# Kernel tuning notes

Hardware: AMD Instinct MI355X
Metric: run time of the kernel (lower is better)

Reference implementation:

```python
import jax, jax.numpy as jnp
import numpy as np

BETA = 0.25

def _l2norm(x, eps=1e-12):
    # F.normalize(x, dim=-1)
    n = jnp.sqrt(jnp.sum(x * x, axis=-1, keepdims=True))
    return x / jnp.maximum(n, eps)

def setup_inputs() -> dict:
    key = jax.random.key(0)
    k1, k2 = jax.random.split(key)
    z = jax.random.normal(k1, (32, 1024, 32), dtype=jnp.float32)
    embedding = jax.random.normal(k2, (8192, 32), dtype=jnp.float32)
    return {"z": z, "embedding": embedding}

def reference(z, embedding):
    B, T, D = z.shape
    zf = _l2norm(z.reshape(-1, D))            # [N, D]
    en = _l2norm(embedding)                   # [n_e, D]
    # squared distances: ||z||^2 + ||e||^2 - 2 z.e  -> [N, n_e]
    d = (jnp.sum(zf * zf, axis=1, keepdims=True)
         + jnp.sum(en * en, axis=1)
         - 2.0 * jnp.einsum('nd,kd->nk', zf, en))
    idx = jnp.argmin(d, axis=1).reshape(B, T)            # [B, T]
    z_q = embedding[idx]                                  # [B, T, D] gather
    z_qnorm = _l2norm(z_q)
    z_norm = _l2norm(z)
    loss = (BETA * jnp.mean((jax.lax.stop_gradient(z_qnorm) - z_norm) ** 2)
            + jnp.mean((z_qnorm - jax.lax.stop_gradient(z_norm)) ** 2))
    # straight-through estimator
    z_q_out = z + jax.lax.stop_gradient(z_qnorm - z)
    return z_q_out, loss, idx
```

## Files before the change

### kernel.cpp

```cpp
#include <hip/hip_runtime.h>
#include <math.h>


#define D 32
#define KCODES 8192
#define MARGIN 2.5e-4f
#define EPS 1e-12f

typedef short bf16x8 __attribute__((ext_vector_type(8)));
typedef unsigned short u16x8 __attribute__((ext_vector_type(8)));
typedef float f32x4 __attribute__((ext_vector_type(4)));

static __device__ __forceinline__ unsigned short f2bf(float x) {
  unsigned u = __float_as_uint(x);
  return (unsigned short)((u + 0x7FFFu + ((u >> 16) & 1u)) >> 16);
}
static __device__ __forceinline__ float bf2f(unsigned short s) {
  return __uint_as_float(((unsigned)s) << 16);
}
static __device__ __forceinline__ void gload_lds16(const void* g, void* l) {
  __builtin_amdgcn_global_load_lds(
      (const __attribute__((address_space(1))) void*)g,
      (__attribute__((address_space(3))) void*)l, 16, 0, 0);
}


__global__ __launch_bounds__(256) void k_prep(const float* __restrict__ z,
                                              const float* __restrict__ emb,
                                              float* __restrict__ en,
                                              float* __restrict__ en_h,
                                              unsigned short* __restrict__ eswz,
                                              unsigned short* __restrict__ zswz_hi,
                                              unsigned short* __restrict__ zswz_lo,
                                              float* __restrict__ zn,
                                              int* __restrict__ cnt,
                                              float* __restrict__ loss,
                                              unsigned long long* __restrict__ mp2,
                                              int N) {
  int v = blockIdx.x * 256 + threadIdx.x;
  if (v == 0) { *cnt = 0; *loss = 0.f; }
  if (v >= KCODES + N) return;
  if (v >= KCODES) mp2[v - KCODES] = 0ull;
  const float* src = (v < KCODES) ? (emb + (size_t)v * D) : (z + (size_t)(v - KCODES) * D);

  float x[D];
  const float4* p = reinterpret_cast<const float4*>(src);
#pragma unroll
  for (int j = 0; j < D / 4; ++j) {
    float4 q = p[j];
    x[4 * j + 0] = q.x; x[4 * j + 1] = q.y; x[4 * j + 2] = q.z; x[4 * j + 3] = q.w;
  }
  float ss = 0.f;
#pragma unroll
  for (int j = 0; j < D; ++j) ss = fmaf(x[j], x[j], ss);
  float n = fmaxf(sqrtf(ss), EPS);
#pragma unroll
  for (int j = 0; j < D; ++j) x[j] = x[j] / n;

  unsigned short hi[D], lo[D];
#pragma unroll
  for (int j = 0; j < D; ++j) {
    hi[j] = f2bf(x[j]);
    lo[j] = f2bf(x[j] - bf2f(hi[j]));
  }

  if (v < KCODES) {
    float4* o = reinterpret_cast<float4*>(en + (size_t)v * D);
    float s2 = 0.f;
#pragma unroll
    for (int j = 0; j < D / 4; ++j) {
      float4 q = {x[4 * j], x[4 * j + 1], x[4 * j + 2], x[4 * j + 3]};
      s2 = fmaf(q.x, q.x, fmaf(q.y, q.y, fmaf(q.z, q.z, fmaf(q.w, q.w, s2))));
      o[j] = q;
    }
    en_h[v] = 0.5f * s2;
    int tl = v >> 4, m = v & 15;
#pragma unroll
    for (int q = 0; q < 4; ++q) {
      u16x8 hv, lv;
#pragma unroll
      for (int j = 0; j < 8; ++j) { hv[j] = hi[8 * q + j]; lv[j] = lo[8 * q + j]; }
      *(u16x8*)(eswz + (size_t)tl * 1024 + (q * 16 + m) * 8) = hv;
      *(u16x8*)(eswz + (size_t)tl * 1024 + 512 + (q * 16 + m) * 8) = lv;
    }
  } else {
    int r = v - KCODES;
    float4* zo = reinterpret_cast<float4*>(zn + (size_t)r * D);
#pragma unroll
    for (int j = 0; j < D / 4; ++j) {
      float4 q = {x[4 * j], x[4 * j + 1], x[4 * j + 2], x[4 * j + 3]};
      zo[j] = q;
    }
    int g = r >> 4, m = r & 15;
#pragma unroll
    for (int q = 0; q < 4; ++q) {
      u16x8 hv, lv;
#pragma unroll
      for (int j = 0; j < 8; ++j) { hv[j] = hi[8 * q + j]; lv[j] = lo[8 * q + j]; }
      *(u16x8*)(zswz_hi + (size_t)g * 512 + (q * 16 + m) * 8) = hv;
      *(u16x8*)(zswz_lo + (size_t)g * 512 + (q * 16 + m) * 8) = lv;
    }
  }
}

__global__ __launch_bounds__(256, 4) void k_argmin_mfma(
    const unsigned short* __restrict__ zswz_hi,
    const unsigned short* __restrict__ zswz_lo,
    const unsigned short* __restrict__ eswz,
    float* __restrict__ res_s1, int* __restrict__ res_cb,
    float* __restrict__ res_s2) {
  __shared__ unsigned short lds_sh[2][8192];

  const int tid = threadIdx.x;
  const int wid = tid >> 6, lane = tid & 63;
  const int lane15 = lane & 15, quad = lane >> 4;
  const int rs = blockIdx.x >> 2;
  const int qt = blockIdx.x & 3;

  bf16x8 zhi[4], zlo[4];
#pragma unroll
  for (int rg = 0; rg < 4; ++rg) {
    int g = rs * 16 + wid * 4 + rg;
    zhi[rg] = *(const bf16x8*)(zswz_hi + (size_t)g * 512 + lane * 8);
    zlo[rg] = *(const bf16x8*)(zswz_lo + (size_t)g * 512 + lane * 8);
  }

  float cm[4], s1g[4], s2c[4];
  int cb[4];
#pragma unroll
  for (int rg = 0; rg < 4; ++rg) {
    cm[rg] = -3.4e38f; s1g[rg] = -3.4e38f; s2c[rg] = -3.4e38f; cb[rg] = 0;
  }
  const f32x4 zero4 = {0.f, 0.f, 0.f, 0.f};

  const float4* gall = reinterpret_cast<const float4*>(eswz) + (size_t)qt * 16 * 1024;
#pragma unroll
  for (int i = 0; i < 4; ++i) {
    int off = i * 256 + tid;
    gload_lds16(gall + off, (char*)&lds_sh[0][0] + (size_t)off * 16);
  }

  for (int c = 0; c < 16; ++c) {
    __syncthreads();
    if (c + 1 < 16) {
      const float4* gn = gall + (size_t)(c + 1) * 1024;
      char* dst = (char*)&lds_sh[(c + 1) & 1][0];
#pragma unroll
      for (int i = 0; i < 4; ++i) {
        int off = i * 256 + tid;
        gload_lds16(gn + off, dst + (size_t)off * 16);
      }
    }
    const unsigned short* buf = &lds_sh[c & 1][0];
#pragma unroll
    for (int t = 0; t < 8; ++t) {
      bf16x8 ahi = *(const bf16x8*)(buf + t * 1024 + lane * 8);
      bf16x8 alo = *(const bf16x8*)(buf + t * 1024 + 512 + lane * 8);
#pragma unroll
      for (int rg = 0; rg < 4; ++rg) {
        f32x4 acc = __builtin_amdgcn_mfma_f32_16x16x32_bf16(ahi, zhi[rg], zero4, 0, 0, 0);
        acc = __builtin_amdgcn_mfma_f32_16x16x32_bf16(ahi, zlo[rg], acc, 0, 0, 0);
        acc = __builtin_amdgcn_mfma_f32_16x16x32_bf16(alo, zhi[rg], acc, 0, 0, 0);
        cm[rg] = fmaxf(cm[rg],
                       fmaxf(fmaxf(acc[0], acc[1]), fmaxf(acc[2], acc[3])));
      }
    }
#pragma unroll
    for (int rg = 0; rg < 4; ++rg) {
      float old1 = s1g[rg];
      s2c[rg] = fmaxf(s2c[rg], fminf(cm[rg], old1));
      bool better = cm[rg] > old1;
      cb[rg] = better ? ((qt * 16 + c) >> 1) : cb[rg];
      s1g[rg] = better ? cm[rg] : old1;
      cm[rg] = -3.4e38f;
    }
  }

#pragma unroll
  for (int m = 16; m <= 32; m <<= 1) {
#pragma unroll
    for (int rg = 0; rg < 4; ++rg) {
      float o1 = __shfl_xor(s1g[rg], m, 64);
      float o2 = __shfl_xor(s2c[rg], m, 64);
      int ob = __shfl_xor(cb[rg], m, 64);
      s2c[rg] = fmaxf(fmaxf(s2c[rg], o2), fminf(s1g[rg], o1));
      bool better = o1 > s1g[rg];
      s1g[rg] = better ? o1 : s1g[rg];
      cb[rg] = better ? ob : cb[rg];
    }
  }
  if (quad == 0) {
#pragma unroll
    for (int rg = 0; rg < 4; ++rg) {
      int row = rs * 256 + wid * 64 + rg * 16 + lane15;
      res_s1[(size_t)row * 4 + qt] = s1g[rg];
      res_cb[(size_t)row * 4 + qt] = cb[rg];
      res_s2[(size_t)row * 4 + qt] = s2c[rg];
    }
  }
}

__global__ __launch_bounds__(256) void k_rescore(
    const float* __restrict__ zn, const float* __restrict__ en,
    const float* __restrict__ en_h,
    const float* __restrict__ res_s1, const int* __restrict__ res_cb,
    const float* __restrict__ res_s2,
    int* __restrict__ idx_ws, int* __restrict__ list, int* __restrict__ cnt,
    int N) {
  __shared__ float en_s[256 * 36];
  __shared__ float enh_s[256];
  __shared__ unsigned short rows_s[2048];
  __shared__ int nmatch;

  const int tid = threadIdx.x;
  const int c = blockIdx.x >> 4;
  const int sb = blockIdx.x & 15;
  const int rows_per = N >> 4;
  const int r0 = sb * rows_per;

  if (tid == 0) nmatch = 0;
  const float4* e4 = reinterpret_cast<const float4*>(en) + (size_t)c * 2048;
#pragma unroll
  for (int i = 0; i < 8; ++i) {
    int idx = i * 256 + tid;
    float4 v4 = e4[idx];
    int code = idx >> 3, j = idx & 7;
    *reinterpret_cast<float4*>(&en_s[code * 36 + j * 4]) = v4;
  }
  enh_s[tid] = en_h[c * 256 + tid];
  __syncthreads();

  for (int i = 0; i < rows_per / 256; ++i) {
    int rrel = i * 256 + tid;
    int row = r0 + rrel;
    float4 s1q = reinterpret_cast<const float4*>(res_s1)[row];
    int4 cbq = reinterpret_cast<const int4*>(res_cb)[row];
    float s1b = s1q.x;  int cbb = cbq.x;
    if (s1q.y > s1b) { s1b = s1q.y; cbb = cbq.y; }
    if (s1q.z > s1b) { s1b = s1q.z; cbb = cbq.z; }
    if (s1q.w > s1b) { s1b = s1q.w; cbb = cbq.w; }
    if (cbb == c) {
      int pos = atomicAdd(&nmatch, 1);
      rows_s[pos] = (unsigned short)rrel;
    }
  }
  __syncthreads();
  const int nm = nmatch;
  const int lane = tid & 63, wid = tid >> 6;

  for (int ri = wid; ri < nm; ri += 4) {
    int rrel = (int)rows_s[ri];
    int row = __builtin_amdgcn_readfirstlane(r0 + rrel);
    const float* znr = zn + (size_t)row * D;
    float v[D];
#pragma unroll
    for (int d = 0; d < D; ++d) v[d] = znr[d];

    unsigned long long best = 0ull;
#pragma unroll
    for (int cc = 0; cc < 4; ++cc) {
      int kl = lane + cc * 64;
      float a = -enh_s[kl];
      const float* ep = &en_s[kl * 36];
#pragma unroll
      for (int jj = 0; jj < 8; ++jj) {
        float4 e = *reinterpret_cast<const float4*>(&ep[jj * 4]);
        a = fmaf(v[4 * jj + 0], e.x, a);
        a = fmaf(v[4 * jj + 1], e.y, a);
        a = fmaf(v[4 * jj + 2], e.z, a);
        a = fmaf(v[4 * jj + 3], e.w, a);
      }
      int k = c * 256 + kl;
      unsigned o = __float_as_uint(a);
      o = (o & 0x80000000u) ? ~o : (o | 0x80000000u);
      unsigned long long pk = ((unsigned long long)o << 32) | (unsigned)(8191 - k);
      best = (pk > best) ? pk : best;
    }
#pragma unroll
    for (int m = 32; m >= 1; m >>= 1) {
      unsigned long long op = __shfl_xor(best, m, 64);
      best = (op > best) ? op : best;
    }
    if (lane == 0) {
      unsigned uo = (unsigned)(best >> 32);
      unsigned uu = (uo & 0x80000000u) ? (uo & 0x7FFFFFFFu) : ~uo;
      float sC = __uint_as_float(uu);
      int kC = 8191 - (int)(unsigned)(best & 0xFFFFFFFFull);
      float dotw = sC + enh_s[kC - c * 256];
      float4 s1q = reinterpret_cast<const float4*>(res_s1)[row];
      float4 s2q = reinterpret_cast<const float4*>(res_s2)[row];
      float hi1 = fmaxf(s1q.x, s1q.y), lo1 = fminf(s1q.x, s1q.y);
      float hi2 = fmaxf(s1q.z, s1q.w), lo2 = fminf(s1q.z, s1q.w);
      float m2 = fmaxf(fminf(hi1, hi2), fmaxf(lo1, lo2));
      float s2all = fmaxf(fmaxf(fmaxf(s2q.x, s2q.y), fmaxf(s2q.z, s2q.w)), m2);
      if (s2all > dotw - MARGIN) {
        int pos = atomicAdd(cnt, 1);
        list[pos] = row;
        idx_ws[row] = -(pos + 1);
      } else {
        idx_ws[row] = kC;
      }
    }
  }
}

__global__ __launch_bounds__(256) void k_cleanup(const float* __restrict__ zn,
                                                 const float* __restrict__ en,
                                                 const float* __restrict__ en_h,
                                                 const int* __restrict__ list,
                                                 const int* __restrict__ cnt,
                                                 unsigned long long* __restrict__ mp2) {
  __shared__ unsigned long long wred[4];
  const int tid = threadIdx.x;
  const int lane = tid & 63, wid = tid >> 6;
  const int ntask = (*cnt) * 32;

  for (int j = blockIdx.x; j < ntask; j += gridDim.x) {
    int i = j >> 5, kc = j & 31;
    int row = list[i];
    const float* znr = zn + (size_t)row * D;
    float v[D];
#pragma unroll
    for (int d = 0; d < D; ++d) v[d] = znr[d];

    int k = kc * 256 + tid;
    const float4* er = reinterpret_cast<const float4*>(en + (size_t)k * D);
    float a = -en_h[k];
#pragma unroll
    for (int jj = 0; jj < 8; ++jj) {
      float4 e = er[jj];
      a = fmaf(v[4 * jj + 0], e.x, a);
      a = fmaf(v[4 * jj + 1], e.y, a);
      a = fmaf(v[4 * jj + 2], e.z, a);
      a = fmaf(v[4 * jj + 3], e.w, a);
    }
    unsigned o = __float_as_uint(a);
    o = (o & 0x80000000u) ? ~o : (o | 0x80000000u);
    unsigned long long pk = ((unsigned long long)o << 32) | (unsigned)(8191 - k);
#pragma unroll
    for (int m = 32; m >= 1; m >>= 1) {
      unsigned long long op = __shfl_xor(pk, m, 64);
      pk = (op > pk) ? op : pk;
    }
    if (lane == 0) wred[wid] = pk;
    __syncthreads();
    if (tid == 0) {
      unsigned long long m01 = (wred[0] > wred[1]) ? wred[0] : wred[1];
      unsigned long long m23 = (wred[2] > wred[3]) ? wred[2] : wred[3];
      atomicMax(&mp2[i], (m01 > m23) ? m01 : m23);
    }
    __syncthreads();
  }
}

__global__ __launch_bounds__(256) void k_epi(const float* __restrict__ z,
                                             const float* __restrict__ en,
                                             const int* __restrict__ idx_ws,
                                             const unsigned long long* __restrict__ mp2,
                                             float* __restrict__ out_z,
                                             float* __restrict__ loss,
                                             float* __restrict__ out_idx,
                                             float scale) {
  int row = blockIdx.x * 256 + threadIdx.x;
  int kb = idx_ws[row];
  if (kb < 0) {
    unsigned long long m = mp2[-kb - 1];
    kb = 8191 - (int)(unsigned)(m & 0xFFFFFFFFull);
  }
  out_idx[row] = (float)kb;

  const float4* p = reinterpret_cast<const float4*>(z + (size_t)row * D);
  float4 q[D / 4];
#pragma unroll
  for (int j = 0; j < D / 4; ++j) q[j] = p[j];
  float ss = 0.f;
#pragma unroll
  for (int j = 0; j < D / 4; ++j)
    ss = fmaf(q[j].x, q[j].x, fmaf(q[j].y, q[j].y, fmaf(q[j].z, q[j].z, fmaf(q[j].w, q[j].w, ss))));
  float n = fmaxf(sqrtf(ss), EPS);

  const float4* ep = reinterpret_cast<const float4*>(en + (size_t)kb * D);
  float4* op = reinterpret_cast<float4*>(out_z + (size_t)row * D);
  float s = 0.f;
#pragma unroll
  for (int j = 0; j < D / 4; ++j) {
    float4 e = ep[j];
    float4 o;
    o.x = q[j].x + (e.x - q[j].x);
    o.y = q[j].y + (e.y - q[j].y);
    o.z = q[j].z + (e.z - q[j].z);
    o.w = q[j].w + (e.w - q[j].w);
    op[j] = o;
    float dx = e.x - q[j].x / n;  float dy = e.y - q[j].y / n;
    float dz = e.z - q[j].z / n;  float dw = e.w - q[j].w / n;
    s = fmaf(dx, dx, fmaf(dy, dy, fmaf(dz, dz, fmaf(dw, dw, s))));
  }

#pragma unroll
  for (int off = 32; off > 0; off >>= 1) s += __shfl_down(s, off, 64);
  __shared__ float wsum[4];
  int lane = threadIdx.x & 63, wid = threadIdx.x >> 6;
  if (lane == 0) wsum[wid] = s;
  __syncthreads();
  if (threadIdx.x == 0) {
    float tt = (wsum[0] + wsum[1]) + (wsum[2] + wsum[3]);
    atomicAdd(loss, tt * scale);
  }
}

extern "C" void kernel_launch(void* const* d_in, const int* in_sizes, int n_in,
                              void* d_out, int out_size, void* d_ws, size_t ws_size,
                              hipStream_t stream) {
  const float* z = (const float*)d_in[0];
  const float* emb = (const float*)d_in[1];
  const int N = in_sizes[0] / D;
  const int K = in_sizes[1] / D;

  float* out = (float*)d_out;
  float* out_z = out;
  float* loss = out + (size_t)N * D;
  float* out_idx = out + (size_t)N * D + 1;

  float* zn = out_z;

  char* w = (char*)d_ws;
  float* en = (float*)w;                         w += (size_t)K * D * 4;
  float* en_h = (float*)w;                       w += (size_t)K * 4;
  unsigned short* eswz = (unsigned short*)w;     w += (size_t)K * D * 2 * 2;
  unsigned short* zswz_hi = (unsigned short*)w;  w += (size_t)N * D * 2;
  unsigned short* zswz_lo = (unsigned short*)w;  w += (size_t)N * D * 2;
  int* idx_ws = (int*)w;                         w += (size_t)N * 4;
  int* list = (int*)w;                           w += (size_t)N * 4;
  unsigned long long* mp2 = (unsigned long long*)w; w += (size_t)N * 8;
  float* res_s1 = (float*)w;                     w += (size_t)N * 4 * 4;
  int* res_cb = (int*)w;                         w += (size_t)N * 4 * 4;
  float* res_s2 = (float*)w;                     w += (size_t)N * 4 * 4;
  int* cnt = (int*)w;

  k_prep<<<dim3((K + N) / 256), 256, 0, stream>>>(
      z, emb, en, en_h, eswz, zswz_hi, zswz_lo, zn, cnt, loss, mp2, N);

  k_argmin_mfma<<<dim3((N / 256) * 4), 256, 0, stream>>>(
      zswz_hi, zswz_lo, eswz, res_s1, res_cb, res_s2);

  k_rescore<<<dim3(32 * 16), 256, 0, stream>>>(
      zn, en, en_h, res_s1, res_cb, res_s2, idx_ws, list, cnt, N);

  k_cleanup<<<dim3(4096), 256, 0, stream>>>(zn, en, en_h, list, cnt, mp2);

  k_epi<<<dim3(N / 256), 256, 0, stream>>>(
      z, en, idx_ws, mp2, out_z, loss, out_idx, 1.25f / (float)((size_t)N * D));
}
```

Baseline: 174.4 us.

## Load codebook fragments directly from global memory instead of LDS double buffer

Drops the LDS double-buffered staging of the swizzled codebook (global_load_lds plus __syncthreads) and has each wave read its bf16 A fragments straight from global memory (L2/L1 cached). The chunk loop is regrouped into 8 chunks of 16 tiles so the coarse codebook-block index stays consistent. It removes block-wide barriers and the LDS footprint, and lowers the launch-bounds occupancy hint from 4 to 2 blocks, which gives more registers per thread. The trade-off is that all four waves now fetch the same codebook data redundantly through the cache, and the load latency is no longer hidden by explicit prefetching.

```diff
diff --git a/kernel.cpp b/kernel.cpp
--- a/kernel.cpp
+++ b/kernel.cpp
@@ -17,11 +17,6 @@
 }
 static __device__ __forceinline__ float bf2f(unsigned short s) {
   return __uint_as_float(((unsigned)s) << 16);
-}
-static __device__ __forceinline__ void gload_lds16(const void* g, void* l) {
-  __builtin_amdgcn_global_load_lds(
-      (const __attribute__((address_space(1))) void*)g,
-      (__attribute__((address_space(3))) void*)l, 16, 0, 0);
 }
 
 
@@ -103,14 +98,12 @@
   }
 }
 
-__global__ __launch_bounds__(256, 4) void k_argmin_mfma(
+__global__ __launch_bounds__(256, 2) void k_argmin_mfma(
     const unsigned short* __restrict__ zswz_hi,
     const unsigned short* __restrict__ zswz_lo,
     const unsigned short* __restrict__ eswz,
     float* __restrict__ res_s1, int* __restrict__ res_cb,
     float* __restrict__ res_s2) {
-  __shared__ unsigned short lds_sh[2][8192];
-
   const int tid = threadIdx.x;
   const int wid = tid >> 6, lane = tid & 63;
   const int lane15 = lane & 15, quad = lane >> 4;
@@ -133,29 +126,14 @@
   }
   const f32x4 zero4 = {0.f, 0.f, 0.f, 0.f};
 
-  const float4* gall = reinterpret_cast<const float4*>(eswz) + (size_t)qt * 16 * 1024;
-#pragma unroll
-  for (int i = 0; i < 4; ++i) {
-    int off = i * 256 + tid;
-    gload_lds16(gall + off, (char*)&lds_sh[0][0] + (size_t)off * 16);
-  }
-
-  for (int c = 0; c < 16; ++c) {
-    __syncthreads();
-    if (c + 1 < 16) {
-      const float4* gn = gall + (size_t)(c + 1) * 1024;
-      char* dst = (char*)&lds_sh[(c + 1) & 1][0];
-#pragma unroll
-      for (int i = 0; i < 4; ++i) {
-        int off = i * 256 + tid;
-        gload_lds16(gn + off, dst + (size_t)off * 16);
-      }
-    }
-    const unsigned short* buf = &lds_sh[c & 1][0];
-#pragma unroll
-    for (int t = 0; t < 8; ++t) {
-      bf16x8 ahi = *(const bf16x8*)(buf + t * 1024 + lane * 8);
-      bf16x8 alo = *(const bf16x8*)(buf + t * 1024 + 512 + lane * 8);
+  const unsigned short* ebase = eswz + (size_t)qt * 128 * 1024 + lane * 8;
+
+  for (int c = 0; c < 8; ++c) {
+#pragma unroll
+    for (int t2 = 0; t2 < 16; ++t2) {
+      const unsigned short* pt = ebase + (size_t)(c * 16 + t2) * 1024;
+      bf16x8 ahi = *(const bf16x8*)pt;
+      bf16x8 alo = *(const bf16x8*)(pt + 512);
 #pragma unroll
       for (int rg = 0; rg < 4; ++rg) {
         f32x4 acc = __builtin_amdgcn_mfma_f32_16x16x32_bf16(ahi, zhi[rg], zero4, 0, 0, 0);
@@ -170,7 +148,7 @@
       float old1 = s1g[rg];
       s2c[rg] = fmaxf(s2c[rg], fminf(cm[rg], old1));
       bool better = cm[rg] > old1;
-      cb[rg] = better ? ((qt * 16 + c) >> 1) : cb[rg];
+      cb[rg] = better ? (qt * 8 + c) : cb[rg];
       s1g[rg] = better ? cm[rg] : old1;
       cm[rg] = -3.4e38f;
     }
```

Measured after the change: 195.1 us. 1.12x slower.
